# Kernel optimization log

Measured on AMD Instinct MI355X. Metric: run time of the kernel, lower is better.

Reference implementation:

```python
import jax, jax.numpy as jnp
import numpy as np

B, D, H, NE = 16, 64, 768, 7  # batch, max_doc_len, bert hidden, n_emotion
FEAT = H + NE + 1             # 776; pair dim = 2*FEAT = 1552

def setup_inputs() -> dict:
    key = jax.random.key(0)
    ks = jax.random.split(key, 8)
    s = lambda k, shp, fan: jax.random.normal(k, shp, jnp.float32) / np.sqrt(fan)
    return {
        "pooled_output": jax.random.normal(ks[0], (B * D, H), jnp.float32),
        "speaker_ids": jax.random.randint(ks[1], (B, D), 0, 2, jnp.int64),
        "emo_w": s(ks[2], (H, NE), H),
        "emo_b": jnp.zeros((NE,), jnp.float32),
        "gate_w": s(ks[3], (2 * FEAT, 2), 2 * FEAT),
        "gate_b": jnp.zeros((2,), jnp.float32),
        "exp_w1": s(ks[4], (2, 2 * FEAT, 256), 2 * FEAT),
        "exp_b1": jnp.zeros((2, 256), jnp.float32),
        "exp_w2": s(ks[5], (2, 256, 2), 256),
        "exp_b2": jnp.zeros((2, 2), jnp.float32),
    }

def reference(pooled_output, speaker_ids, emo_w, emo_b, gate_w, gate_b, exp_w1, exp_b1, exp_w2, exp_b2):
    # emotion head (dropout is identity in eval)
    emotion_pred = pooled_output @ emo_w + emo_b                      # [B*D, 7]
    # concatenated per-utterance embedding [B, D, FEAT]
    spk = speaker_ids.reshape(-1, 1).astype(pooled_output.dtype)
    conc = jnp.concatenate([pooled_output, emotion_pred, spk], axis=1).reshape(B, D, FEAT)
    # vectorized pair build: (t, end_t) with t <= end_t, end_t-major order
    idx_end, idx_t = np.tril_indices(D)                               # P = D*(D+1)/2
    pair = jnp.concatenate([conc[:, idx_t], conc[:, idx_end]], axis=-1)  # [B, P, 2*FEAT]
    flat = pair.reshape(-1, 2 * FEAT)                                 # [N, 1552]
    # gating (detached input, guiding_lambda = 0 so no subtask label term)
    gating = jax.lax.stop_gradient(flat) @ gate_w + gate_b            # [N, 2]
    # soft-gated expert combine
    h = jnp.einsum('nf,efh->enh', flat, exp_w1) + exp_b1[:, None, :]  # [E, N, 256]
    o = jnp.einsum('enh,ehc->enc', h, exp_w2) + exp_b2[:, None, :]    # [E, N, 2]
    cause_pred = jnp.einsum('enc,ne->nc', o, gating)                  # [N, 2]
    return emotion_pred, cause_pred
```

## Files before the change

### kernel.cpp

```cpp
#include <hip/hip_runtime.h>


#define H_     768
#define NE_    7
#define FEAT_  776
#define TWOF   1552
#define NROW   1024
#define PAIRS  2080
#define NPAIR  33280
#define EXH    256

#define M_OFF  0
#define BC_OFF 6208
#define PC_OFF 6212

__global__ __launch_bounds__(256) void kM(const float* __restrict__ w1,
                                          const float* __restrict__ b1,
                                          const float* __restrict__ w2,
                                          const float* __restrict__ b2,
                                          float* __restrict__ M,
                                          float* __restrict__ bc) {
    const int lane = threadIdx.x & 63;
    const int wave = threadIdx.x >> 6;
    const int blk  = blockIdx.x;

    int e, r = 0;
    float4 a;
    if (blk < 776) {
        const int row = blk * 4 + wave;
        e = row / TWOF;
        r = row - e * TWOF;
        a = ((const float4*)(w1 + ((size_t)e * TWOF + r) * EXH))[lane];
    } else {
        if (wave >= 2) return;
        e = wave;
        a = ((const float4*)(b1 + e * EXH))[lane];
    }

    const float4* wv = (const float4*)(w2 + (size_t)e * EXH * 2);
    const float4 q0 = wv[lane * 2];
    const float4 q1 = wv[lane * 2 + 1];
    float a0 = a.x * q0.x + a.y * q0.z + a.z * q1.x + a.w * q1.z;
    float a1 = a.x * q0.y + a.y * q0.w + a.z * q1.y + a.w * q1.w;

#pragma unroll
    for (int off = 32; off; off >>= 1) {
        a0 += __shfl_down(a0, off);
        a1 += __shfl_down(a1, off);
    }
    if (lane == 0) {
        if (blk < 776) {
            M[((size_t)e * TWOF + r) * 2 + 0] = a0;
            M[((size_t)e * TWOF + r) * 2 + 1] = a1;
        } else {
            bc[e * 2 + 0] = a0 + b2[e * 2 + 0];
            bc[e * 2 + 1] = a1 + b2[e * 2 + 1];
        }
    }
}

__global__ __launch_bounds__(256) void kRow(const float* __restrict__ pooled,
                                            const int* __restrict__ spk,
                                            const float* __restrict__ emo_w,
                                            const float* __restrict__ emo_b,
                                            const float* __restrict__ gate_w,
                                            const float* __restrict__ M,
                                            float* __restrict__ out_emo,
                                            float* __restrict__ pc) {
    __shared__ __align__(16) float conc[FEAT_];
    __shared__ float redE[4][NE_];
    __shared__ float redP[4][12];

    const int row  = blockIdx.x;
    const int t    = threadIdx.x;
    const int lane = t & 63;
    const int wave = t >> 6;

    float acc[NE_] = {0.f, 0.f, 0.f, 0.f, 0.f, 0.f, 0.f};
    if (t < 192) {
        const float4 c4 = *(const float4*)(pooled + (size_t)row * H_ + 4 * t);
        *(float4*)(conc + 4 * t) = c4;
        const float* ew = emo_w + (size_t)(4 * t) * NE_;
#pragma unroll
        for (int k = 0; k < NE_; k++)
            acc[k] = c4.x * ew[k] + c4.y * ew[NE_ + k] +
                     c4.z * ew[2 * NE_ + k] + c4.w * ew[3 * NE_ + k];
    }
#pragma unroll
    for (int off = 32; off; off >>= 1)
#pragma unroll
        for (int k = 0; k < NE_; k++) acc[k] += __shfl_down(acc[k], off);
    if (lane == 0)
#pragma unroll
        for (int k = 0; k < NE_; k++) redE[wave][k] = acc[k];
    __syncthreads();

    if (t < NE_) {
        const float v = emo_b[t] + redE[0][t] + redE[1][t] + redE[2][t] + redE[3][t];
        out_emo[row * NE_ + t] = v;
        conc[H_ + t] = v;
    } else if (t == NE_) {
        conc[FEAT_ - 1] = (float)spk[row];
    }
    __syncthreads();

    float pa[12] = {0.f, 0.f, 0.f, 0.f, 0.f, 0.f, 0.f, 0.f, 0.f, 0.f, 0.f, 0.f};
    if (t < 194) {
        const float4 c4 = *(const float4*)(conc + 4 * t);
#pragma unroll
        for (int half = 0; half < 2; ++half) {
#pragma unroll
            for (int e = 0; e < 2; ++e) {
                const float* mb = M + ((size_t)e * TWOF + half * FEAT_ + 4 * t) * 2;
                const float4 v0 = *(const float4*)mb;
                const float4 v1 = *(const float4*)(mb + 4);
                const int j = half * 4 + e * 2;
                pa[j]     += c4.x * v0.x + c4.y * v0.z + c4.z * v1.x + c4.w * v1.z;
                pa[j + 1] += c4.x * v0.y + c4.y * v0.w + c4.z * v1.y + c4.w * v1.w;
            }
            const float* gb = gate_w + ((size_t)half * FEAT_ + 4 * t) * 2;
            const float4 g0 = *(const float4*)gb;
            const float4 g1 = *(const float4*)(gb + 4);
            pa[8 + half * 2]     += c4.x * g0.x + c4.y * g0.z + c4.z * g1.x + c4.w * g1.z;
            pa[8 + half * 2 + 1] += c4.x * g0.y + c4.y * g0.w + c4.z * g1.y + c4.w * g1.w;
        }
    }
#pragma unroll
    for (int off = 32; off; off >>= 1)
#pragma unroll
        for (int k = 0; k < 12; k++) pa[k] += __shfl_down(pa[k], off);
    if (lane == 0)
#pragma unroll
        for (int k = 0; k < 12; k++) redP[wave][k] = pa[k];
    __syncthreads();

    if (t < 12)
        pc[row * 12 + t] = redP[0][t] + redP[1][t] + redP[2][t] + redP[3][t];
}

__global__ __launch_bounds__(256) void kPair(const float* __restrict__ pc,
                                             const float* __restrict__ bc,
                                             const float* __restrict__ gate_b,
                                             float* __restrict__ out_cause) {
    const int n = blockIdx.x * 256 + threadIdx.x;
    if (n >= NPAIR) return;
    const int b = n / PAIRS;
    const int p = n - b * PAIRS;

    int end = (int)((sqrtf(8.0f * (float)p + 1.0f) - 1.0f) * 0.5f);
    while ((end + 1) * (end + 2) / 2 <= p) end++;
    while (end * (end + 1) / 2 > p) end--;
    const int tt = p - end * (end + 1) / 2;

    const float* pt = pc + ((size_t)b * 64 + tt) * 12;
    const float* pe = pc + ((size_t)b * 64 + end) * 12;

    const float g0 = pt[8] + pe[10] + gate_b[0];
    const float g1 = pt[9] + pe[11] + gate_b[1];

    const float o00 = pt[0] + pe[4] + bc[0];
    const float o01 = pt[1] + pe[5] + bc[1];
    const float o10 = pt[2] + pe[6] + bc[2];
    const float o11 = pt[3] + pe[7] + bc[3];

    out_cause[(size_t)n * 2 + 0] = o00 * g0 + o10 * g1;
    out_cause[(size_t)n * 2 + 1] = o01 * g0 + o11 * g1;
}

extern "C" void kernel_launch(void* const* d_in, const int* in_sizes, int n_in,
                              void* d_out, int out_size, void* d_ws, size_t ws_size,
                              hipStream_t stream) {
    const float* pooled = (const float*)d_in[0];
    const int*   spk    = (const int*)d_in[1];
    const float* emo_w  = (const float*)d_in[2];
    const float* emo_b  = (const float*)d_in[3];
    const float* gate_w = (const float*)d_in[4];
    const float* gate_b = (const float*)d_in[5];
    const float* exp_w1 = (const float*)d_in[6];
    const float* exp_b1 = (const float*)d_in[7];
    const float* exp_w2 = (const float*)d_in[8];
    const float* exp_b2 = (const float*)d_in[9];

    float* out = (float*)d_out;
    float* W   = (float*)d_ws;
    float* M   = W + M_OFF;
    float* bc  = W + BC_OFF;
    float* pc  = W + PC_OFF;

    hipLaunchKernelGGL(kM, dim3(777), dim3(256), 0, stream,
                       exp_w1, exp_b1, exp_w2, exp_b2, M, bc);
    hipLaunchKernelGGL(kRow, dim3(NROW), dim3(256), 0, stream,
                       pooled, spk, emo_w, emo_b, gate_w, M, out, pc);
    hipLaunchKernelGGL(kPair, dim3((NPAIR + 255) / 256), dim3(256), 0, stream,
                       pc, bc, gate_b, out + NROW * NE_);
}
```

Baseline: 18.47 us.

## Move emotion head into weight-fold kernel and drop row-kernel syncs

The emotion-head matvec moves into the first kernel as extra blocks, one wave per row, so it runs alongside the expert-weight fold. The per-row projection kernel then reads pooled data and the precomputed emotion/speaker values straight from global memory, removing the shared-memory staging and two block barriers. Per-row partials are padded to 16 floats so the pair kernel can use float4 loads. In exchange the emotion row is read twice from global memory, and the wave-per-row emotion loop uses scalar, less-coalesced emo_w loads.

```diff
diff --git a/kernel.cpp b/kernel.cpp
--- a/kernel.cpp
+++ b/kernel.cpp
@@ -10,65 +10,90 @@
 #define NPAIR  33280
 #define EXH    256
 
-#define M_OFF  0
-#define BC_OFF 6208
-#define PC_OFF 6212
-
-__global__ __launch_bounds__(256) void kM(const float* __restrict__ w1,
-                                          const float* __restrict__ b1,
-                                          const float* __restrict__ w2,
-                                          const float* __restrict__ b2,
-                                          float* __restrict__ M,
-                                          float* __restrict__ bc) {
+#define M_OFF   0
+#define BC_OFF  6208
+#define EMO_OFF 6212
+#define PC_OFF  14404
+
+__global__ __launch_bounds__(256) void kPre(const float* __restrict__ w1,
+                                            const float* __restrict__ b1,
+                                            const float* __restrict__ w2,
+                                            const float* __restrict__ b2,
+                                            const float* __restrict__ pooled,
+                                            const int* __restrict__ spk,
+                                            const float* __restrict__ emo_w,
+                                            const float* __restrict__ emo_b,
+                                            float* __restrict__ W,
+                                            float* __restrict__ out_emo) {
     const int lane = threadIdx.x & 63;
     const int wave = threadIdx.x >> 6;
     const int blk  = blockIdx.x;
 
-    int e, r = 0;
-    float4 a;
-    if (blk < 776) {
-        const int row = blk * 4 + wave;
-        e = row / TWOF;
-        r = row - e * TWOF;
-        a = ((const float4*)(w1 + ((size_t)e * TWOF + r) * EXH))[lane];
-    } else {
-        if (wave >= 2) return;
-        e = wave;
-        a = ((const float4*)(b1 + e * EXH))[lane];
-    }
-
-    const float4* wv = (const float4*)(w2 + (size_t)e * EXH * 2);
-    const float4 q0 = wv[lane * 2];
-    const float4 q1 = wv[lane * 2 + 1];
-    float a0 = a.x * q0.x + a.y * q0.z + a.z * q1.x + a.w * q1.z;
-    float a1 = a.x * q0.y + a.y * q0.w + a.z * q1.y + a.w * q1.w;
-
-#pragma unroll
-    for (int off = 32; off; off >>= 1) {
-        a0 += __shfl_down(a0, off);
-        a1 += __shfl_down(a1, off);
-    }
+    if (blk < 777) {
+        int e, r = 0;
+        float4 a;
+        if (blk < 776) {
+            const int row = blk * 4 + wave;
+            e = row / TWOF;
+            r = row - e * TWOF;
+            a = ((const float4*)(w1 + ((size_t)e * TWOF + r) * EXH))[lane];
+        } else {
+            if (wave >= 2) return;
+            e = wave;
+            a = ((const float4*)(b1 + e * EXH))[lane];
+        }
+        const float4* wv = (const float4*)(w2 + (size_t)e * EXH * 2);
+        const float4 q0 = wv[lane * 2];
+        const float4 q1 = wv[lane * 2 + 1];
+        float a0 = a.x * q0.x + a.y * q0.z + a.z * q1.x + a.w * q1.z;
+        float a1 = a.x * q0.y + a.y * q0.w + a.z * q1.y + a.w * q1.w;
+#pragma unroll
+        for (int off = 32; off; off >>= 1) {
+            a0 += __shfl_down(a0, off);
+            a1 += __shfl_down(a1, off);
+        }
+        if (lane == 0) {
+            if (blk < 776) {
+                W[M_OFF + ((size_t)e * TWOF + r) * 2 + 0] = a0;
+                W[M_OFF + ((size_t)e * TWOF + r) * 2 + 1] = a1;
+            } else {
+                W[BC_OFF + e * 2 + 0] = a0 + b2[e * 2 + 0];
+                W[BC_OFF + e * 2 + 1] = a1 + b2[e * 2 + 1];
+            }
+        }
+        return;
+    }
+
+    const int row = (blk - 777) * 4 + wave;
+    const float* pr = pooled + (size_t)row * H_;
+    float acc[NE_] = {0.f, 0.f, 0.f, 0.f, 0.f, 0.f, 0.f};
+#pragma unroll
+    for (int i = 0; i < 12; ++i) {
+        const float p = pr[lane + 64 * i];
+        const float* ew = emo_w + (size_t)(lane + 64 * i) * NE_;
+#pragma unroll
+        for (int k = 0; k < NE_; ++k) acc[k] += p * ew[k];
+    }
+#pragma unroll
+    for (int off = 32; off; off >>= 1)
+#pragma unroll
+        for (int k = 0; k < NE_; ++k) acc[k] += __shfl_down(acc[k], off);
     if (lane == 0) {
-        if (blk < 776) {
-            M[((size_t)e * TWOF + r) * 2 + 0] = a0;
-            M[((size_t)e * TWOF + r) * 2 + 1] = a1;
-        } else {
-            bc[e * 2 + 0] = a0 + b2[e * 2 + 0];
-            bc[e * 2 + 1] = a1 + b2[e * 2 + 1];
-        }
-    }
-}
-
-__global__ __launch_bounds__(256) void kRow(const float* __restrict__ pooled,
-                                            const int* __restrict__ spk,
-                                            const float* __restrict__ emo_w,
-                                            const float* __restrict__ emo_b,
-                                            const float* __restrict__ gate_w,
-                                            const float* __restrict__ M,
-                                            float* __restrict__ out_emo,
-                                            float* __restrict__ pc) {
-    __shared__ __align__(16) float conc[FEAT_];
-    __shared__ float redE[4][NE_];
+        float* er = W + EMO_OFF + (size_t)row * 8;
+#pragma unroll
+        for (int k = 0; k < NE_; ++k) {
+            const float v = acc[k] + emo_b[k];
+            out_emo[(size_t)row * NE_ + k] = v;
+            er[k] = v;
+        }
+        er[7] = (float)spk[row];
+    }
+}
+
+__global__ __launch_bounds__(256) void kProj(const float* __restrict__ pooled,
+                                             const float* __restrict__ gate_w,
+                                             const float* __restrict__ W,
+                                             float* __restrict__ pc) {
     __shared__ float redP[4][12];
 
     const int row  = blockIdx.x;
@@ -76,37 +101,16 @@
     const int lane = t & 63;
     const int wave = t >> 6;
 
-    float acc[NE_] = {0.f, 0.f, 0.f, 0.f, 0.f, 0.f, 0.f};
+    float4 c4 = {0.f, 0.f, 0.f, 0.f};
     if (t < 192) {
-        const float4 c4 = *(const float4*)(pooled + (size_t)row * H_ + 4 * t);
-        *(float4*)(conc + 4 * t) = c4;
-        const float* ew = emo_w + (size_t)(4 * t) * NE_;
-#pragma unroll
-        for (int k = 0; k < NE_; k++)
-            acc[k] = c4.x * ew[k] + c4.y * ew[NE_ + k] +
-                     c4.z * ew[2 * NE_ + k] + c4.w * ew[3 * NE_ + k];
-    }
-#pragma unroll
-    for (int off = 32; off; off >>= 1)
-#pragma unroll
-        for (int k = 0; k < NE_; k++) acc[k] += __shfl_down(acc[k], off);
-    if (lane == 0)
-#pragma unroll
-        for (int k = 0; k < NE_; k++) redE[wave][k] = acc[k];
-    __syncthreads();
-
-    if (t < NE_) {
-        const float v = emo_b[t] + redE[0][t] + redE[1][t] + redE[2][t] + redE[3][t];
-        out_emo[row * NE_ + t] = v;
-        conc[H_ + t] = v;
-    } else if (t == NE_) {
-        conc[FEAT_ - 1] = (float)spk[row];
-    }
-    __syncthreads();
+        c4 = *(const float4*)(pooled + (size_t)row * H_ + 4 * t);
+    } else if (t < 194) {
+        c4 = *(const float4*)(W + EMO_OFF + (size_t)row * 8 + (t - 192) * 4);
+    }
 
     float pa[12] = {0.f, 0.f, 0.f, 0.f, 0.f, 0.f, 0.f, 0.f, 0.f, 0.f, 0.f, 0.f};
     if (t < 194) {
-        const float4 c4 = *(const float4*)(conc + 4 * t);
+        const float* M = W + M_OFF;
 #pragma unroll
         for (int half = 0; half < 2; ++half) {
 #pragma unroll
@@ -128,14 +132,14 @@
 #pragma unroll
     for (int off = 32; off; off >>= 1)
 #pragma unroll
-        for (int k = 0; k < 12; k++) pa[k] += __shfl_down(pa[k], off);
+        for (int k = 0; k < 12; ++k) pa[k] += __shfl_down(pa[k], off);
     if (lane == 0)
 #pragma unroll
-        for (int k = 0; k < 12; k++) redP[wave][k] = pa[k];
+        for (int k = 0; k < 12; ++k) redP[wave][k] = pa[k];
     __syncthreads();
 
     if (t < 12)
-        pc[row * 12 + t] = redP[0][t] + redP[1][t] + redP[2][t] + redP[3][t];
+        pc[(size_t)row * 16 + t] = redP[0][t] + redP[1][t] + redP[2][t] + redP[3][t];
 }
 
 __global__ __launch_bounds__(256) void kPair(const float* __restrict__ pc,
@@ -152,16 +156,20 @@
     while (end * (end + 1) / 2 > p) end--;
     const int tt = p - end * (end + 1) / 2;
 
-    const float* pt = pc + ((size_t)b * 64 + tt) * 12;
-    const float* pe = pc + ((size_t)b * 64 + end) * 12;
-
-    const float g0 = pt[8] + pe[10] + gate_b[0];
-    const float g1 = pt[9] + pe[11] + gate_b[1];
-
-    const float o00 = pt[0] + pe[4] + bc[0];
-    const float o01 = pt[1] + pe[5] + bc[1];
-    const float o10 = pt[2] + pe[6] + bc[2];
-    const float o11 = pt[3] + pe[7] + bc[3];
+    const float* pt = pc + ((size_t)b * 64 + tt) * 16;
+    const float* pe = pc + ((size_t)b * 64 + end) * 16;
+    const float4 u0 = *(const float4*)pt;
+    const float4 u2 = *(const float4*)(pt + 8);
+    const float4 v1 = *(const float4*)(pe + 4);
+    const float4 v2 = *(const float4*)(pe + 8);
+
+    const float g0 = u2.x + v2.z + gate_b[0];
+    const float g1 = u2.y + v2.w + gate_b[1];
+
+    const float o00 = u0.x + v1.x + bc[0];
+    const float o01 = u0.y + v1.y + bc[1];
+    const float o10 = u0.z + v1.z + bc[2];
+    const float o11 = u0.w + v1.w + bc[3];
 
     out_cause[(size_t)n * 2 + 0] = o00 * g0 + o10 * g1;
     out_cause[(size_t)n * 2 + 1] = o01 * g0 + o11 * g1;
@@ -183,14 +191,12 @@
 
     float* out = (float*)d_out;
     float* W   = (float*)d_ws;
-    float* M   = W + M_OFF;
-    float* bc  = W + BC_OFF;
-    float* pc  = W + PC_OFF;
-
-    hipLaunchKernelGGL(kM, dim3(777), dim3(256), 0, stream,
-                       exp_w1, exp_b1, exp_w2, exp_b2, M, bc);
-    hipLaunchKernelGGL(kRow, dim3(NROW), dim3(256), 0, stream,
-                       pooled, spk, emo_w, emo_b, gate_w, M, out, pc);
+
+    hipLaunchKernelGGL(kPre, dim3(1033), dim3(256), 0, stream,
+                       exp_w1, exp_b1, exp_w2, exp_b2,
+                       pooled, spk, emo_w, emo_b, W, out);
+    hipLaunchKernelGGL(kProj, dim3(NROW), dim3(256), 0, stream,
+                       pooled, gate_w, W, W + PC_OFF);
     hipLaunchKernelGGL(kPair, dim3((NPAIR + 255) / 256), dim3(256), 0, stream,
-                       pc, bc, gate_b, out + NROW * NE_);
-}
+                       W + PC_OFF, W + BC_OFF, gate_b, out + NROW * NE_);
+}
```

After: 17.24 us, median of 2. 1.07x faster.
